# Performance work log

Measured on AMD Instinct MI355X. Metric: run time of the kernel, lower is better.

Reference implementation:

```python
import jax, jax.numpy as jnp
import numpy as np

BETA = 0.2
EPS = 1e-10
N_LAYERS = 5  # same shared-weight gconv applied 5 times


def setup_inputs() -> dict:
    key = jax.random.key(0)
    ks = jax.random.split(key, 5)
    B, J, C = 16384, 17, 128
    x = jax.random.normal(ks[0], (B, J, C), dtype=jnp.float32)
    x0 = jax.random.normal(ks[1], (B, J, C), dtype=jnp.float32)
    adj = jax.random.uniform(ks[2], (J, J), dtype=jnp.float32)
    adj = 0.5 * (adj + adj.T)  # symmetric skeleton-like adjacency
    W0 = jax.random.normal(ks[3], (C, C), dtype=jnp.float32) * (1.0 / np.sqrt(C))
    W1 = jax.random.normal(ks[4], (C, C), dtype=jnp.float32) * (1.0 / np.sqrt(C))
    b = jnp.zeros((C,), dtype=jnp.float32)
    gamma = jnp.ones((C,), dtype=jnp.float32)
    beta_ln = jnp.zeros((C,), dtype=jnp.float32)
    return {"x": x, "x0": x0, "adj": adj, "W0": W0, "W1": W1, "b": b,
            "gamma": gamma, "beta_ln": beta_ln}


def _gconv(x, x0, adj_diag, adj_off, W0, W1, b):
    # self-loop term uses W0, neighbor aggregation uses W1
    h0 = jnp.einsum('bjc,cd->bjd', x, W0)
    h1 = jnp.einsum('bjc,cd->bjd', x, W1)
    out = adj_diag[None, :, None] * h0 + jnp.einsum('jk,bkd->bjd', adj_off, h1)
    return BETA * x0 + (1.0 - BETA) * out + b


def _layernorm(x, gamma, beta_ln):
    mu = jnp.mean(x, axis=-1, keepdims=True)
    var = jnp.mean(jnp.square(x - mu), axis=-1, keepdims=True)
    return (x - mu) * jax.lax.rsqrt(var + EPS) * gamma + beta_ln


def reference(x, x0, adj, W0, W1, b, gamma, beta_ln):
    J = adj.shape[0]
    eye = jnp.eye(J, dtype=adj.dtype)
    adj_diag = jnp.diagonal(adj)          # [J] self-loop weights
    adj_off = adj * (1.0 - eye)           # [J,J] neighbor weights
    for _ in range(N_LAYERS):
        x = _gconv(x, x0, adj_diag, adj_off, W0, W1, b)
    return _layernorm(x, gamma, beta_ln)
```

## Files before the change

kernel.cpp:

```cpp
#include <hip/hip_runtime.h>
#include <stdint.h>

typedef unsigned short u16;
typedef unsigned int   u32;
typedef _Float16 f16x8 __attribute__((ext_vector_type(8)));
typedef __attribute__((ext_vector_type(16))) float f16v;

#define JJ 17
#define CC 128
#define BB 7
#define ROWS (BB*JJ)
#define PP 128
#define XP 132
#define HTP 140
#define NLAYERS 5
#define NT 1024

#define XH_OFF   0
#define HT_OFF   33792
#define W_OFF    69632
#define DIAG_OFF 137216
#define LDS_BYTES (DIAG_OFF + 512)

#define MFMA __builtin_amdgcn_mfma_f32_32x32x16_f16

__device__ __forceinline__ u16 h2b(_Float16 h) {
  union { _Float16 h; u16 b; } c; c.h = h; return c.b;
}
__device__ __forceinline__ _Float16 b2h(u16 b) {
  union { u16 b; _Float16 h; } c; c.b = b; return c.h;
}
__device__ __forceinline__ float wred(float v) {
  #pragma unroll
  for (int m = 32; m >= 1; m >>= 1) v += __shfl_xor(v, m, 64);
  return v;
}
__device__ __forceinline__ f16x8 u4f8(uint4 v) {
  union { uint4 u; f16x8 f; } c; c.u = v; return c.f;
}
__device__ __forceinline__ f16x8 mk8(uint2 a, uint2 b) {
  union { uint4 u; f16x8 f; } c;
  c.u.x = a.x; c.u.y = a.y; c.u.z = b.x; c.u.w = b.y;
  return c.f;
}

__global__ void __launch_bounds__(256)
wprep(const float* __restrict__ W0, const float* __restrict__ W1,
      const float* __restrict__ adj, u16* __restrict__ wsH,
      u16* __restrict__ amixf)
{
  __shared__ float wt[64*130];
  const int w01 = blockIdx.x;
  const float* Wp = w01 ? W1 : W0;
  const int tid = threadIdx.x;
  if (w01 == 0) {
    for (int t = tid; t < 8192; t += 256) {
      int e  = t & 7, nl = (t >> 3) & 31, g = (t >> 8) & 1;
      int i  = (t >> 9) & 3, tt = t >> 11;
      const int kslo = (tt==0)?0:(tt==1)?1:(tt==2)?3:4;
      int row = tt*32 + nl;
      int k   = (kslo + i)*16 + 8*g + e;
      float v = 0.f;
      if (row < ROWS && k < ROWS && (row/JJ) == (k/JJ) && (row%JJ) != (k%JJ))
        v = 0.8f * adj[(row%JJ)*JJ + (k%JJ)];
      amixf[t] = h2b((_Float16)v);
    }
  }
  for (int kh = 0; kh < 2; ++kh) {
    if (kh) __syncthreads();
    #pragma unroll
    for (int i = 0; i < 32; ++i) {
      int idx = tid + i*256;
      int kk = idx >> 7, col = idx & 127;
      wt[kk*130 + col] = Wp[(kh*64 + kk)*128 + col];
    }
    __syncthreads();
    #pragma unroll
    for (int i = 0; i < 32; ++i) {
      int idx = tid + i*256;
      int col = idx >> 6, kk = idx & 63;
      wsH[(size_t)(w01*128 + col)*128 + kh*64 + kk] = h2b((_Float16)wt[kk*130 + col]);
    }
  }
}

__global__ void __launch_bounds__(NT, 4)
gconv_fused(const float* __restrict__ x, const float* __restrict__ x0,
            const float* __restrict__ adj, const u16* __restrict__ wsH,
            const u16* __restrict__ amixf, const float* __restrict__ bvec,
            const float* __restrict__ gamma, const float* __restrict__ beta,
            float* __restrict__ out, int totRows)
{
  extern __shared__ char smem[];
  u16*   xh    = (u16*)(smem + XH_OFF);
  u16*   h1t   = (u16*)(smem + HT_OFF);
  u16*   wlds  = (u16*)(smem + W_OFF);
  float* diag8 = (float*)(smem + DIAG_OFF);

  const int tid  = threadIdx.x;
  const int lane = tid & 63;
  const int wid  = tid >> 6;
  const int wm   = wid >> 2;
  const int wn   = wid & 3;
  const int g    = lane >> 5;
  const int nl   = lane & 31;
  const int ccol = wn*32 + nl;
  const int grow0 = blockIdx.x * ROWS;
  const int kslo = (wm==0)?0:(wm==1)?1:(wm==2)?3:4;

  {
    int el = tid * 32;
    int w01 = el >> 14, rem = el & 16383;
    int col = rem >> 7, k0 = rem & 127;
    const u16* src = wsH + el;
    u16* dst = &wlds[(w01*128 + col)*XP + k0];
    #pragma unroll
    for (int c = 0; c < 8; ++c)
      *(uint2*)(dst + c*4) = *(const uint2*)(src + c*4);
  }

  u32 x0p[8];
  #pragma unroll
  for (int qp = 0; qp < 8; ++qp) {
    u32 pk = 0;
    #pragma unroll
    for (int h = 0; h < 2; ++h) {
      int q = qp*2 + h;
      int row = wm*32 + (q&3) + 8*(q>>2) + 4*g;
      int grow = grow0 + row;
      u16 bits = 0;
      if (row < ROWS && grow < totRows)
        bits = h2b((_Float16)(0.2f * x0[(size_t)grow*CC + ccol]));
      pk |= ((u32)bits) << (16*h);
    }
    x0p[qp] = pk;
  }
  const float bias_c = bvec[ccol];

  #pragma unroll
  for (int i = 0; i < 4; ++i) {
    int el4 = tid + i*NT;
    int r = el4 >> 5, c4 = (el4 & 31) << 2;
    float4 v = make_float4(0.f, 0.f, 0.f, 0.f);
    if (r < ROWS && (grow0 + r) < totRows)
      v = *(const float4*)&x[(size_t)(grow0 + r)*CC + c4];
    u16 s0 = h2b((_Float16)v.x), s1 = h2b((_Float16)v.y);
    u16 s2 = h2b((_Float16)v.z), s3 = h2b((_Float16)v.w);
    *(uint2*)&xh[r*XP + c4] = make_uint2((u32)s0 | ((u32)s1<<16), (u32)s2 | ((u32)s3<<16));
  }
  if (tid >= 512 && tid < 512 + PP) {
    int t = tid - 512;
    int j = t % JJ;
    diag8[t] = (t < ROWS) ? 0.8f * adj[j*JJ + j] : 0.f;
  }
  __syncthreads();

  const int arow = (wm*32 + nl)*XP;
  const int bb0  = ccol*XP;
  const int bb1  = bb0 + 128*XP;
  const u16* amp = amixf + ((wm*4*2) + g)*256 + nl*8;

  #pragma unroll 1
  for (int layer = 0; layer < NLAYERS; ++layer) {
    f16v acc0, acc1;
    #pragma unroll
    for (int i = 0; i < 16; ++i) { acc0[i] = 0.f; acc1[i] = 0.f; }

    #pragma unroll
    for (int ks = 0; ks < 8; ++ks) {
      const int o = ks*16 + 8*g;
      f16x8 ah = mk8(*(const uint2*)&xh[arow + o],  *(const uint2*)&xh[arow + o + 4]);
      f16x8 b0 = mk8(*(const uint2*)&wlds[bb0 + o], *(const uint2*)&wlds[bb0 + o + 4]);
      f16x8 b1 = mk8(*(const uint2*)&wlds[bb1 + o], *(const uint2*)&wlds[bb1 + o + 4]);
      acc0 = MFMA(ah, b0, acc0, 0, 0, 0);
      acc1 = MFMA(ah, b1, acc1, 0, 0, 0);
      __builtin_amdgcn_sched_barrier(0);
    }

    #pragma unroll
    for (int qp = 0; qp < 8; ++qp) {
      int q = qp*2;
      int row = wm*32 + (q&3) + 8*(q>>2) + 4*g;
      u32 pk = (u32)h2b((_Float16)acc1[q]) | ((u32)h2b((_Float16)acc1[q+1]) << 16);
      *(u32*)&h1t[ccol*HTP + row] = pk;
    }
    __syncthreads();

    #pragma unroll
    for (int i = 0; i < 16; ++i) acc1[i] = 0.f;
    #pragma unroll
    for (int i = 0; i < 4; ++i) {
      f16x8 am = u4f8(*(const uint4*)(amp + i*512));
      const int hidx = ccol*HTP + (kslo + i)*16 + 8*g;
      f16x8 hb = mk8(*(const uint2*)&h1t[hidx], *(const uint2*)&h1t[hidx+4]);
      acc1 = MFMA(am, hb, acc1, 0, 0, 0);
    }

    #pragma unroll
    for (int q = 0; q < 16; ++q) {
      int row = wm*32 + (q&3) + 8*(q>>2) + 4*g;
      float x0v = (float)b2h((u16)(x0p[q>>1] >> (16*(q&1))));
      float v = x0v + diag8[row]*acc0[q] + acc1[q] + bias_c;
      xh[row*XP + ccol] = h2b((_Float16)v);
    }
    __syncthreads();
  }

  float ga = gamma[lane], g2 = gamma[64+lane];
  float ba = beta[lane],  b2f = beta[64+lane];
  #pragma unroll 1
  for (int i = 0; i < 8; ++i) {
    int r = wid + 16*i;
    if (r >= ROWS) continue;
    int grow = grow0 + r;
    if (grow >= totRows) continue;
    float xa = (float)b2h(xh[r*XP + lane]);
    float xc = (float)b2h(xh[r*XP + 64 + lane]);
    float mu = wred(xa + xc) * (1.f/128.f);
    float da = xa - mu, dc = xc - mu;
    float vs = wred(da*da + dc*dc) * (1.f/128.f);
    float rs = rsqrtf(vs + 1e-10f);
    size_t ob = (size_t)grow*CC;
    out[ob + lane]      = da*rs*ga + ba;
    out[ob + 64 + lane] = dc*rs*g2 + b2f;
  }
}

extern "C" void kernel_launch(void* const* d_in, const int* in_sizes, int n_in,
                              void* d_out, int out_size, void* d_ws, size_t ws_size,
                              hipStream_t stream) {
  const float* x   = (const float*)d_in[0];
  const float* x0  = (const float*)d_in[1];
  const float* adj = (const float*)d_in[2];
  const float* W0  = (const float*)d_in[3];
  const float* W1  = (const float*)d_in[4];
  const float* bv  = (const float*)d_in[5];
  const float* ga  = (const float*)d_in[6];
  const float* be  = (const float*)d_in[7];
  u16* wsH   = (u16*)d_ws;
  u16* amixf = (u16*)((char*)d_ws + 65536);
  int totRows = in_sizes[0] / CC;
  int nBatch  = totRows / JJ;
  int grid    = (nBatch + BB - 1) / BB;
  wprep<<<dim3(2), dim3(256), 0, stream>>>(W0, W1, adj, wsH, amixf);
  hipFuncSetAttribute((const void*)gconv_fused,
                      hipFuncAttributeMaxDynamicSharedMemorySize, LDS_BYTES);
  gconv_fused<<<dim3(grid), dim3(NT), LDS_BYTES, stream>>>(
      x, x0, adj, wsH, amixf, bv, ga, be, (float*)d_out, totRows);
}
```

Baseline: 374.1 us.

## Stream MFMA weight fragments from global in fragment order instead of LDS

Weights are pre-swizzled by the prep kernel into MFMA B-fragment order, so each lane reads them directly from global/L2 with 16-byte loads that are software-prefetched one k-step ahead. The LDS copy of both weight matrices is dropped. Blocks shrink to 3 batches (51 rows) and 512 threads, which brings LDS to about 34 KB and allows more resident blocks per CU. In exchange the 128-row M tile is underused by more padding and each layer re-reads the weights from cache instead of LDS.

After: 390.4 us. 4.4% more time.

```diff
diff --git a/kernel.cpp b/kernel.cpp
--- a/kernel.cpp
+++ b/kernel.cpp
@@ -8,19 +8,18 @@
 
 #define JJ 17
 #define CC 128
-#define BB 7
+#define BB 3
 #define ROWS (BB*JJ)
-#define PP 128
+#define PP 64
 #define XP 132
-#define HTP 140
+#define HTP 68
 #define NLAYERS 5
-#define NT 1024
+#define NT 512
 
 #define XH_OFF   0
-#define HT_OFF   33792
-#define W_OFF    69632
-#define DIAG_OFF 137216
-#define LDS_BYTES (DIAG_OFF + 512)
+#define HT_OFF   16896
+#define DIAG_OFF 34304
+#define LDS_BYTES (DIAG_OFF + 256)
 
 #define MFMA __builtin_amdgcn_mfma_f32_32x32x16_f16
 
@@ -46,7 +45,7 @@
 
 __global__ void __launch_bounds__(256)
 wprep(const float* __restrict__ W0, const float* __restrict__ W1,
-      const float* __restrict__ adj, u16* __restrict__ wsH,
+      const float* __restrict__ adj, u16* __restrict__ ws2,
       u16* __restrict__ amixf)
 {
   __shared__ float wt[64*130];
@@ -54,10 +53,10 @@
   const float* Wp = w01 ? W1 : W0;
   const int tid = threadIdx.x;
   if (w01 == 0) {
-    for (int t = tid; t < 8192; t += 256) {
+    for (int t = tid; t < 2*3*2*256; t += 256) {
       int e  = t & 7, nl = (t >> 3) & 31, g = (t >> 8) & 1;
-      int i  = (t >> 9) & 3, tt = t >> 11;
-      const int kslo = (tt==0)?0:(tt==1)?1:(tt==2)?3:4;
+      int i  = (t >> 9) % 3, tt = t / 1536;
+      const int kslo = tt;
       int row = tt*32 + nl;
       int k   = (kslo + i)*16 + 8*g + e;
       float v = 0.f;
@@ -78,15 +77,17 @@
     #pragma unroll
     for (int i = 0; i < 32; ++i) {
       int idx = tid + i*256;
-      int col = idx >> 6, kk = idx & 63;
-      wsH[(size_t)(w01*128 + col)*128 + kh*64 + kk] = h2b((_Float16)wt[kk*130 + col]);
+      int e = idx & 7, col = (idx >> 3) & 127;
+      int g = (idx >> 10) & 1, ksl = idx >> 11;
+      int kk = ksl*16 + 8*g + e;
+      ws2[(size_t)w01*16384 + kh*8192 + idx] = h2b((_Float16)wt[kk*130 + col]);
     }
   }
 }
 
 __global__ void __launch_bounds__(NT, 4)
 gconv_fused(const float* __restrict__ x, const float* __restrict__ x0,
-            const float* __restrict__ adj, const u16* __restrict__ wsH,
+            const float* __restrict__ adj, const u16* __restrict__ ws2,
             const u16* __restrict__ amixf, const float* __restrict__ bvec,
             const float* __restrict__ gamma, const float* __restrict__ beta,
             float* __restrict__ out, int totRows)
@@ -94,7 +95,6 @@
   extern __shared__ char smem[];
   u16*   xh    = (u16*)(smem + XH_OFF);
   u16*   h1t   = (u16*)(smem + HT_OFF);
-  u16*   wlds  = (u16*)(smem + W_OFF);
   float* diag8 = (float*)(smem + DIAG_OFF);
 
   const int tid  = threadIdx.x;
@@ -106,18 +106,7 @@
   const int nl   = lane & 31;
   const int ccol = wn*32 + nl;
   const int grow0 = blockIdx.x * ROWS;
-  const int kslo = (wm==0)?0:(wm==1)?1:(wm==2)?3:4;
-
-  {
-    int el = tid * 32;
-    int w01 = el >> 14, rem = el & 16383;
-    int col = rem >> 7, k0 = rem & 127;
-    const u16* src = wsH + el;
-    u16* dst = &wlds[(w01*128 + col)*XP + k0];
-    #pragma unroll
-    for (int c = 0; c < 8; ++c)
-      *(uint2*)(dst + c*4) = *(const uint2*)(src + c*4);
-  }
+  const int kslo = wm;
 
   u32 x0p[8];
   #pragma unroll
@@ -148,17 +137,17 @@
     u16 s2 = h2b((_Float16)v.z), s3 = h2b((_Float16)v.w);
     *(uint2*)&xh[r*XP + c4] = make_uint2((u32)s0 | ((u32)s1<<16), (u32)s2 | ((u32)s3<<16));
   }
-  if (tid >= 512 && tid < 512 + PP) {
-    int t = tid - 512;
+  if (tid >= 256 && tid < 256 + PP) {
+    int t = tid - 256;
     int j = t % JJ;
     diag8[t] = (t < ROWS) ? 0.8f * adj[j*JJ + j] : 0.f;
   }
   __syncthreads();
 
   const int arow = (wm*32 + nl)*XP;
-  const int bb0  = ccol*XP;
-  const int bb1  = bb0 + 128*XP;
-  const u16* amp = amixf + ((wm*4*2) + g)*256 + nl*8;
+  const u16* pw0 = ws2 + (size_t)g*1024 + ccol*8;
+  const u16* pw1 = pw0 + 16384;
+  const u16* amp = amixf + ((wm*3*2) + g)*256 + nl*8;
 
   #pragma unroll 1
   for (int layer = 0; layer < NLAYERS; ++layer) {
@@ -166,15 +155,21 @@
     #pragma unroll
     for (int i = 0; i < 16; ++i) { acc0[i] = 0.f; acc1[i] = 0.f; }
 
+    f16x8 b0 = u4f8(*(const uint4*)(pw0));
+    f16x8 b1 = u4f8(*(const uint4*)(pw1));
     #pragma unroll
     for (int ks = 0; ks < 8; ++ks) {
-      const int o = ks*16 + 8*g;
-      f16x8 ah = mk8(*(const uint2*)&xh[arow + o],  *(const uint2*)&xh[arow + o + 4]);
-      f16x8 b0 = mk8(*(const uint2*)&wlds[bb0 + o], *(const uint2*)&wlds[bb0 + o + 4]);
-      f16x8 b1 = mk8(*(const uint2*)&wlds[bb1 + o], *(const uint2*)&wlds[bb1 + o + 4]);
+      f16x8 nb0 = b0, nb1 = b1;
+      if (ks < 7) {
+        nb0 = u4f8(*(const uint4*)(pw0 + (ks+1)*2048));
+        nb1 = u4f8(*(const uint4*)(pw1 + (ks+1)*2048));
+      }
+      const int o = arow + ks*16 + 8*g;
+      f16x8 ah = mk8(*(const uint2*)&xh[o], *(const uint2*)&xh[o+4]);
       acc0 = MFMA(ah, b0, acc0, 0, 0, 0);
       acc1 = MFMA(ah, b1, acc1, 0, 0, 0);
       __builtin_amdgcn_sched_barrier(0);
+      b0 = nb0; b1 = nb1;
     }
 
     #pragma unroll
@@ -189,7 +184,7 @@
     #pragma unroll
     for (int i = 0; i < 16; ++i) acc1[i] = 0.f;
     #pragma unroll
-    for (int i = 0; i < 4; ++i) {
+    for (int i = 0; i < 3; ++i) {
       f16x8 am = u4f8(*(const uint4*)(amp + i*512));
       const int hidx = ccol*HTP + (kslo + i)*16 + 8*g;
       f16x8 hb = mk8(*(const uint2*)&h1t[hidx], *(const uint2*)&h1t[hidx+4]);
@@ -209,8 +204,8 @@
   float ga = gamma[lane], g2 = gamma[64+lane];
   float ba = beta[lane],  b2f = beta[64+lane];
   #pragma unroll 1
-  for (int i = 0; i < 8; ++i) {
-    int r = wid + 16*i;
+  for (int i = 0; i < 7; ++i) {
+    int r = wid + 8*i;
     if (r >= ROWS) continue;
     int grow = grow0 + r;
     if (grow >= totRows) continue;
@@ -237,14 +232,12 @@
   const float* bv  = (const float*)d_in[5];
   const float* ga  = (const float*)d_in[6];
   const float* be  = (const float*)d_in[7];
-  u16* wsH   = (u16*)d_ws;
+  u16* ws2   = (u16*)d_ws;
   u16* amixf = (u16*)((char*)d_ws + 65536);
   int totRows = in_sizes[0] / CC;
   int nBatch  = totRows / JJ;
   int grid    = (nBatch + BB - 1) / BB;
-  wprep<<<dim3(2), dim3(256), 0, stream>>>(W0, W1, adj, wsH, amixf);
-  hipFuncSetAttribute((const void*)gconv_fused,
-                      hipFuncAttributeMaxDynamicSharedMemorySize, LDS_BYTES);
+  wprep<<<dim3(2), dim3(256), 0, stream>>>(W0, W1, adj, ws2, amixf);
   gconv_fused<<<dim3(grid), dim3(NT), LDS_BYTES, stream>>>(
-      x, x0, adj, wsH, amixf, bv, ga, be, (float*)d_out, totRows);
-}
+      x, x0, adj, ws2, amixf, bv, ga, be, (float*)d_out, totRows);
+}
```
